# Performance work log

Measured on AMD Instinct MI355X. Metric: run time of the kernel, lower is better.

The kernel has to match this reference:

```python
import jax, jax.numpy as jnp
import numpy as np

D_MODEL = 1024
N_HEADS = 16
D_HEAD = D_MODEL // N_HEADS
D_FF = 4096
EPS = 1e-5


def layernorm(x, gamma, beta):
    mu = jnp.mean(x, axis=-1, keepdims=True)
    var = jnp.var(x, axis=-1, keepdims=True)
    return (x - mu) * jax.lax.rsqrt(var + EPS) * gamma + beta


def setup_inputs() -> dict:
    key = jax.random.key(0)
    ks = jax.random.split(key, 16)
    B, T = 4, 2048
    s = 1.0 / np.sqrt(D_MODEL)
    sf = 1.0 / np.sqrt(D_FF)
    return {
        "x": jax.random.normal(ks[0], (B, T, D_MODEL), jnp.float32),
        "gate_score": jax.random.uniform(ks[1], (B,), jnp.float32),
        "Wq": jax.random.normal(ks[2], (D_MODEL, D_MODEL), jnp.float32) * s,
        "bq": jnp.zeros((D_MODEL,), jnp.float32),
        "Wk": jax.random.normal(ks[3], (D_MODEL, D_MODEL), jnp.float32) * s,
        "bk": jnp.zeros((D_MODEL,), jnp.float32),
        "Wv": jax.random.normal(ks[4], (D_MODEL, D_MODEL), jnp.float32) * s,
        "bv": jnp.zeros((D_MODEL,), jnp.float32),
        "Wo": jax.random.normal(ks[5], (D_MODEL, D_MODEL), jnp.float32) * s,
        "bo": jnp.zeros((D_MODEL,), jnp.float32),
        "W1": jax.random.normal(ks[6], (D_MODEL, D_FF), jnp.float32) * s,
        "b1": jnp.zeros((D_FF,), jnp.float32),
        "W2": jax.random.normal(ks[7], (D_FF, D_MODEL), jnp.float32) * sf,
        "b2": jnp.zeros((D_MODEL,), jnp.float32),
        "gamma1": jnp.ones((D_MODEL,), jnp.float32),
        "beta1": jnp.zeros((D_MODEL,), jnp.float32),
        "gamma2": jnp.ones((D_MODEL,), jnp.float32),
        "beta2": jnp.zeros((D_MODEL,), jnp.float32),
    }


def reference(x, gate_score, Wq, bq, Wk, bk, Wv, bv, Wo, bo,
              W1, b1, W2, b2, gamma1, beta1, gamma2, beta2):
    B, T, C = x.shape
    # --- attention sub-block (pre-norm) ---
    h = layernorm(x, gamma1, beta1)
    Q = (h @ Wq + bq).reshape(B, T, N_HEADS, D_HEAD).transpose(0, 2, 1, 3)
    K = (h @ Wk + bk).reshape(B, T, N_HEADS, D_HEAD).transpose(0, 2, 1, 3)
    V = (h @ Wv + bv).reshape(B, T, N_HEADS, D_HEAD).transpose(0, 2, 1, 3)
    scores = jnp.einsum("bhqd,bhkd->bhqk", Q, K) / np.sqrt(D_HEAD)
    causal = jnp.tril(jnp.ones((T, T), dtype=bool))  # True = keep
    scores = jnp.where(causal, scores, -jnp.inf)
    attn = jax.nn.softmax(scores, axis=-1)
    ctx = jnp.einsum("bhqk,bhkd->bhqd", attn, V)
    ctx = ctx.transpose(0, 2, 1, 3).reshape(B, T, C)
    attn_out = ctx @ Wo + bo
    x1 = x + attn_out
    # --- FFN sub-block (pre-norm) ---
    h2 = layernorm(x1, gamma2, beta2)
    ff = jax.nn.gelu(h2 @ W1 + b1, approximate=False) @ W2 + b2
    x2 = x1 + ff
    # --- gated residual ---
    g = gate_score[:, None, None]
    return x + g * (x2 - x)
```

## Files before the change

### kernel.cpp

```cpp
#include <hip/hip_runtime.h>
#include <hip/hip_bf16.h>
#include <cmath>

typedef unsigned short u16;
typedef __attribute__((ext_vector_type(8))) short short8;
typedef __attribute__((ext_vector_type(4))) float f32x4;

#define DM 1024
#define NH 16
#define DH 64
#define DFF 4096
#define BB 4
#define TT 2048
#define MROWS (BB*TT)

__device__ __forceinline__ float bu2f(u16 u) {
    union { float f; unsigned v; } c; c.v = ((unsigned)u) << 16; return c.f;
}
__device__ __forceinline__ u16 f2bu(float f) {
    __hip_bfloat16 h = __float2bfloat16(f);
    union { __hip_bfloat16 h; u16 u; } c; c.h = h; return c.u;
}
__device__ __forceinline__ void async_copy16(const u16* g, u16* l) {
    __builtin_amdgcn_global_load_lds((const __attribute__((address_space(1))) void*)g,
                                     (__attribute__((address_space(3))) void*)l, 16, 0, 0);
}

__global__ void ln_kernel(const float* __restrict__ x, const float* __restrict__ gamma,
                          const float* __restrict__ beta, u16* __restrict__ out)
{
    int row = blockIdx.x;
    int tid = threadIdx.x;
    float4 v4 = ((const float4*)(x + (size_t)row * DM))[tid];
    float v[4] = { v4.x, v4.y, v4.z, v4.w };
    float s = v[0] + v[1] + v[2] + v[3];
    float ss = v[0]*v[0] + v[1]*v[1] + v[2]*v[2] + v[3]*v[3];
    #pragma unroll
    for (int o = 32; o > 0; o >>= 1) { s += __shfl_down(s, o); ss += __shfl_down(ss, o); }
    __shared__ float red[8];
    int w = tid >> 6;
    if ((tid & 63) == 0) { red[w] = s; red[4 + w] = ss; }
    __syncthreads();
    s  = red[0] + red[1] + red[2] + red[3];
    ss = red[4] + red[5] + red[6] + red[7];
    float mu  = s * (1.0f / DM);
    float var = ss * (1.0f / DM) - mu * mu;
    float rstd = rsqrtf(var + 1e-5f);
    float4 g4 = ((const float4*)gamma)[tid];
    float4 b4 = ((const float4*)beta)[tid];
    float g[4] = { g4.x, g4.y, g4.z, g4.w };
    float b[4] = { b4.x, b4.y, b4.z, b4.w };
    ushort4 o4;
    u16* op = (u16*)&o4;
    #pragma unroll
    for (int i = 0; i < 4; i++) op[i] = f2bu((v[i] - mu) * rstd * g[i] + b[i]);
    ((ushort4*)(out + (size_t)row * DM))[tid] = o4;
}

__global__ void transpose_f2b(const float* __restrict__ in, u16* __restrict__ out,
                              int R, int C)
{
    __shared__ u16 tile[32][33];
    int bx = blockIdx.x * 32;
    int by = blockIdx.y * 32;
    int tx = threadIdx.x, ty = threadIdx.y;
    #pragma unroll
    for (int i = 0; i < 32; i += 8)
        tile[ty + i][tx] = f2bu(in[(size_t)(by + ty + i) * C + bx + tx]);
    __syncthreads();
    #pragma unroll
    for (int i = 0; i < 32; i += 8)
        out[(size_t)(bx + ty + i) * R + by + tx] = tile[tx][ty + i];
}

#define BM 128
#define BN 128
#define BK 32

template<int EPI>
__global__ __launch_bounds__(256, 2) void gemm_bt(
    const u16* __restrict__ A, const u16* __restrict__ Bt,
    const float* __restrict__ bias, void* __restrict__ Cv,
    const float* __restrict__ res, const float* __restrict__ x0,
    const float* __restrict__ gate, int M, int N, int K)
{
    __shared__ __align__(16) u16 As[BM * BK];
    __shared__ __align__(16) u16 Bs[BN * BK];
    int tid = threadIdx.x;
    int lane = tid & 63, wave = tid >> 6;
    int wm = (wave & 1) * 64, wn = (wave >> 1) * 64;
    int lm = lane & 15, quad = lane >> 4;
    size_t row0 = (size_t)blockIdx.x * BM;
    size_t col0 = (size_t)blockIdx.y * BN;

    int sr = tid >> 2;
    int sk = (tid & 3) * 8;
    const u16* Ag = A  + (row0 + sr) * (size_t)K + sk;
    const u16* Bg = Bt + (col0 + sr) * (size_t)K + sk;
    u16* Asl = As + tid * 8;
    u16* Bsl = Bs + tid * 8;

    f32x4 acc[4][4];
    #pragma unroll
    for (int i = 0; i < 4; i++)
        #pragma unroll
        for (int j = 0; j < 4; j++)
            acc[i][j] = (f32x4){0.f, 0.f, 0.f, 0.f};

    for (int k0 = 0; k0 < K; k0 += BK) {
        __syncthreads();
        async_copy16(Ag + k0,                  Asl);
        async_copy16(Ag + (size_t)64 * K + k0, Asl + 64 * BK);
        async_copy16(Bg + k0,                  Bsl);
        async_copy16(Bg + (size_t)64 * K + k0, Bsl + 64 * BK);
        __syncthreads();
        short8 af[4], bfr[4];
        #pragma unroll
        for (int t = 0; t < 4; t++) {
            af[t]  = *(const short8*)&As[(wm + t * 16 + lm) * BK + quad * 8];
            bfr[t] = *(const short8*)&Bs[(wn + t * 16 + lm) * BK + quad * 8];
        }
        #pragma unroll
        for (int mt = 0; mt < 4; mt++)
            #pragma unroll
            for (int nt = 0; nt < 4; nt++)
                acc[mt][nt] = __builtin_amdgcn_mfma_f32_16x16x32_bf16(
                    af[mt], bfr[nt], acc[mt][nt], 0, 0, 0);
    }

    u16*   C16 = (u16*)Cv;
    float* Cf  = (float*)Cv;

    #pragma unroll
    for (int mt = 0; mt < 4; mt++) {
        #pragma unroll
        for (int nt = 0; nt < 4; nt++) {
            #pragma unroll
            for (int r = 0; r < 4; r++) {
                size_t row = row0 + wm + mt * 16 + quad * 4 + r;
                size_t col = col0 + wn + nt * 16 + lm;
                size_t idx = row * (size_t)N + col;
                float v = acc[mt][nt][r] + bias[col];
                if (EPI == 0) {
                    C16[idx] = f2bu(v);
                } else if (EPI == 1) {
                    Cf[idx] = v + res[idx];
                } else if (EPI == 2) {
                    v = 0.5f * v * (1.0f + erff(v * 0.70710678118f));
                    C16[idx] = f2bu(v);
                } else {
                    float xv  = x0[idx];
                    float x1v = res[idx];
                    float g   = gate[row >> 11];
                    Cf[idx] = xv + g * (x1v + v - xv);
                }
            }
        }
    }
}

#define KS 72
#define VS 72

__global__ __launch_bounds__(256, 4) void attn_mfma(
    const u16* __restrict__ Q, const u16* __restrict__ Kg,
    const u16* __restrict__ Vg, u16* __restrict__ ctx)
{
    __shared__ __align__(16) u16 Kl[64][KS];
    __shared__ __align__(16) u16 Vt[80][VS];
    __shared__ __align__(16) u16 Pl[4][32][VS];

    int tid = threadIdx.x, lane = tid & 63, w = tid >> 6;
    int lm = lane & 15, quad = lane >> 4;

    int bi = blockIdx.x;
    int tile = bi & 15, h = (bi >> 4) & 15, b = bi >> 8;
    int q0 = (15 - tile) * 128;
    int qw = q0 + w * 32;

    const size_t hoff = (size_t)h * DH;
    const u16* Qp = Q  + (size_t)b * TT * DM + hoff;
    const u16* Kp = Kg + (size_t)b * TT * DM + hoff;
    const u16* Vp = Vg + (size_t)b * TT * DM + hoff;

    for (int i = tid; i < 16 * VS; i += 256) {
        int r = i / VS, c = i % VS;
        Vt[64 + r][c] = (r == 0 && c < 64) ? (u16)0x3F80 : (u16)0;
    }

    short8 aq[2][2];
    #pragma unroll
    for (int qs = 0; qs < 2; qs++)
        #pragma unroll
        for (int dc = 0; dc < 2; dc++)
            aq[qs][dc] = *(const short8*)(Qp + (size_t)(qw + qs*16 + lm) * DM + dc*32 + quad*8);

    f32x4 o[2][4], o5[2];
    #pragma unroll
    for (int qs = 0; qs < 2; qs++) {
        #pragma unroll
        for (int ds = 0; ds < 4; ds++) o[qs][ds] = (f32x4){0.f, 0.f, 0.f, 0.f};
        o5[qs] = (f32x4){0.f, 0.f, 0.f, 0.f};
    }

    int kkey = tid & 63, kdim = (tid >> 6) * 16;
    int vkey = (tid & 31) * 2, vdim = (tid >> 5) * 8;

    const float sc = 0.18033688011f;
    const float FM = 24.0f;
    int nch = q0 / 64 + 2;

    uint4 kr0 = *(const uint4*)(Kp + (size_t)kkey * DM + kdim);
    uint4 kr1 = *(const uint4*)(Kp + (size_t)kkey * DM + kdim + 8);
    uint4 vr0 = *(const uint4*)(Vp + (size_t)vkey * DM + vdim);
    uint4 vr1 = *(const uint4*)(Vp + (size_t)(vkey + 1) * DM + vdim);

    for (int c = 0; c < nch; c++) {
        int kb = c * 64;
        __syncthreads();
        *(uint4*)&Kl[kkey][kdim]     = kr0;
        *(uint4*)&Kl[kkey][kdim + 8] = kr1;
        {
            const u16* p0 = (const u16*)&vr0;
            const u16* p1 = (const u16*)&vr1;
            #pragma unroll
            for (int j = 0; j < 8; j++) {
                ushort2 pk = { p0[j], p1[j] };
                *(ushort2*)&Vt[vdim + j][vkey] = pk;
            }
        }
        __syncthreads();

        int kbn = (c + 1 < nch) ? kb + 64 : 0;
        kr0 = *(const uint4*)(Kp + (size_t)(kbn + kkey) * DM + kdim);
        kr1 = *(const uint4*)(Kp + (size_t)(kbn + kkey) * DM + kdim + 8);
        vr0 = *(const uint4*)(Vp + (size_t)(kbn + vkey) * DM + vdim);
        vr1 = *(const uint4*)(Vp + (size_t)(kbn + vkey + 1) * DM + vdim);

        if (kb <= qw + 31) {
            f32x4 s[2][4];
            #pragma unroll
            for (int qs = 0; qs < 2; qs++)
                #pragma unroll
                for (int ks = 0; ks < 4; ks++)
                    s[qs][ks] = (f32x4){0.f, 0.f, 0.f, 0.f};
            #pragma unroll
            for (int ks = 0; ks < 4; ks++) {
                short8 b0 = *(const short8*)&Kl[ks * 16 + lm][quad * 8];
                short8 b1 = *(const short8*)&Kl[ks * 16 + lm][32 + quad * 8];
                #pragma unroll
                for (int qs = 0; qs < 2; qs++) {
                    s[qs][ks] = __builtin_amdgcn_mfma_f32_16x16x32_bf16(aq[qs][0], b0, s[qs][ks], 0, 0, 0);
                    s[qs][ks] = __builtin_amdgcn_mfma_f32_16x16x32_bf16(aq[qs][1], b1, s[qs][ks], 0, 0, 0);
                }
            }

            bool maskzone = (kb + 63 > qw);
            #pragma unroll
            for (int qs = 0; qs < 2; qs++)
                #pragma unroll
                for (int ks = 0; ks < 4; ks++)
                    #pragma unroll
                    for (int r = 0; r < 4; r++) {
                        float v = s[qs][ks][r] * sc - FM;
                        if (maskzone && (kb + ks * 16 + lm > qw + qs * 16 + quad * 4 + r))
                            v = -INFINITY;
                        Pl[w][qs * 16 + quad * 4 + r][ks * 16 + lm] = f2bu(exp2f(v));
                    }

            #pragma unroll
            for (int kc = 0; kc < 2; kc++) {
                short8 ap0 = *(const short8*)&Pl[w][lm][kc * 32 + quad * 8];
                short8 ap1 = *(const short8*)&Pl[w][16 + lm][kc * 32 + quad * 8];
                #pragma unroll
                for (int ds = 0; ds < 4; ds++) {
                    short8 bv = *(const short8*)&Vt[ds * 16 + lm][kc * 32 + quad * 8];
                    o[0][ds] = __builtin_amdgcn_mfma_f32_16x16x32_bf16(ap0, bv, o[0][ds], 0, 0, 0);
                    o[1][ds] = __builtin_amdgcn_mfma_f32_16x16x32_bf16(ap1, bv, o[1][ds], 0, 0, 0);
                }
                short8 b5 = *(const short8*)&Vt[64 + lm][kc * 32 + quad * 8];
                o5[0] = __builtin_amdgcn_mfma_f32_16x16x32_bf16(ap0, b5, o5[0], 0, 0, 0);
                o5[1] = __builtin_amdgcn_mfma_f32_16x16x32_bf16(ap1, b5, o5[1], 0, 0, 0);
            }
        }
    }

    #pragma unroll
    for (int qs = 0; qs < 2; qs++) {
        float inv[4];
        #pragma unroll
        for (int r = 0; r < 4; r++)
            inv[r] = 1.0f / __shfl(o5[qs][r], lane & 48);
        #pragma unroll
        for (int ds = 0; ds < 4; ds++)
            #pragma unroll
            for (int r = 0; r < 4; r++) {
                size_t row = (size_t)(b * TT + qw + qs * 16 + quad * 4 + r);
                ctx[row * DM + hoff + ds * 16 + lm] = f2bu(o[qs][ds][r] * inv[r]);
            }
    }
}

extern "C" void kernel_launch(void* const* d_in, const int* in_sizes, int n_in,
                              void* d_out, int out_size, void* d_ws, size_t ws_size,
                              hipStream_t stream)
{
    const float* x    = (const float*)d_in[0];
    const float* gate = (const float*)d_in[1];
    const float* Wq   = (const float*)d_in[2];
    const float* bq   = (const float*)d_in[3];
    const float* Wk   = (const float*)d_in[4];
    const float* bk   = (const float*)d_in[5];
    const float* Wv   = (const float*)d_in[6];
    const float* bv   = (const float*)d_in[7];
    const float* Wo   = (const float*)d_in[8];
    const float* bo   = (const float*)d_in[9];
    const float* W1   = (const float*)d_in[10];
    const float* b1   = (const float*)d_in[11];
    const float* W2   = (const float*)d_in[12];
    const float* b2   = (const float*)d_in[13];
    const float* gamma1 = (const float*)d_in[14];
    const float* beta1  = (const float*)d_in[15];
    const float* gamma2 = (const float*)d_in[16];
    const float* beta2  = (const float*)d_in[17];
    float* out = (float*)d_out;

    char* ws = (char*)d_ws;
    const size_t MB = 1024 * 1024;
    u16* WtQ = (u16*)(ws + 0 * MB);
    u16* WtK = (u16*)(ws + 2 * MB);
    u16* WtV = (u16*)(ws + 4 * MB);
    u16* WtO = (u16*)(ws + 6 * MB);
    u16* Wt1 = (u16*)(ws + 8 * MB);
    u16* Wt2 = (u16*)(ws + 16 * MB);
    u16* h   = (u16*)(ws + 24 * MB);
    u16* ctx = (u16*)(ws + 24 * MB);
    u16* Qb  = (u16*)(ws + 40 * MB);
    u16* Kb  = (u16*)(ws + 56 * MB);
    u16* Vb  = (u16*)(ws + 72 * MB);
    float* x1 = (float*)(ws + 40 * MB);
    u16* h2  = (u16*)(ws + 72 * MB);
    u16* ff  = (u16*)(ws + 88 * MB);

    dim3 tb(32, 8);
    transpose_f2b<<<dim3(DM / 32, DM / 32), tb, 0, stream>>>(Wq, WtQ, DM, DM);
    transpose_f2b<<<dim3(DM / 32, DM / 32), tb, 0, stream>>>(Wk, WtK, DM, DM);
    transpose_f2b<<<dim3(DM / 32, DM / 32), tb, 0, stream>>>(Wv, WtV, DM, DM);
    transpose_f2b<<<dim3(DM / 32, DM / 32), tb, 0, stream>>>(Wo, WtO, DM, DM);
    transpose_f2b<<<dim3(DFF / 32, DM / 32), tb, 0, stream>>>(W1, Wt1, DM, DFF);
    transpose_f2b<<<dim3(DM / 32, DFF / 32), tb, 0, stream>>>(W2, Wt2, DFF, DM);

    ln_kernel<<<MROWS, 256, 0, stream>>>(x, gamma1, beta1, h);

    dim3 gg(MROWS / BM, DM / BN);
    gemm_bt<0><<<gg, 256, 0, stream>>>(h, WtQ, bq, Qb, nullptr, nullptr, nullptr, MROWS, DM, DM);
    gemm_bt<0><<<gg, 256, 0, stream>>>(h, WtK, bk, Kb, nullptr, nullptr, nullptr, MROWS, DM, DM);
    gemm_bt<0><<<gg, 256, 0, stream>>>(h, WtV, bv, Vb, nullptr, nullptr, nullptr, MROWS, DM, DM);

    attn_mfma<<<BB * NH * (TT / 128), 256, 0, stream>>>(Qb, Kb, Vb, ctx);

    gemm_bt<1><<<gg, 256, 0, stream>>>(ctx, WtO, bo, x1, x, nullptr, nullptr, MROWS, DM, DM);

    ln_kernel<<<MROWS, 256, 0, stream>>>(x1, gamma2, beta2, h2);

    gemm_bt<2><<<dim3(MROWS / BM, DFF / BN), 256, 0, stream>>>(h2, Wt1, b1, ff, nullptr, nullptr, nullptr, MROWS, DFF, DM);

    gemm_bt<3><<<gg, 256, 0, stream>>>(ff, Wt2, b2, out, x1, x, gate, MROWS, DM, DFF);
}
```

Before: 631.3 us.

## Fuse QKV projections into one GEMM and rebalance causal attention tiles

Merges the Q, K and V weight transposes and projections into one transpose launch and a single GEMM of width 3*DM writing an interleaved QKV buffer, with per-section bias selection in the epilogue. Attention now reads from the interleaved buffer and gives each block a complementary pair of 64-row query tiles (t and 31-t), so causal work per block is balanced. The softmax denominator now comes from an MFMA against a constant ones vector instead of an extra LDS row, and each wave handles 16 query rows. The GEMM also drops its launch_bounds occupancy hint, which may change register allocation, and the wider strided QKV layout could reduce load locality in attention.

Result: faster. 573.0 us (-9.2%).

```diff
diff --git a/kernel.cpp b/kernel.cpp
--- a/kernel.cpp
+++ b/kernel.cpp
@@ -57,6 +57,26 @@
     ((ushort4*)(out + (size_t)row * DM))[tid] = o4;
 }
 
+__global__ void transpose4_f2b(const float* __restrict__ w0, const float* __restrict__ w1,
+                               const float* __restrict__ w2, const float* __restrict__ w3,
+                               u16* __restrict__ outQKV, u16* __restrict__ outO)
+{
+    __shared__ u16 tile[32][33];
+    const float* in = (blockIdx.z == 0) ? w0 : (blockIdx.z == 1) ? w1
+                     : (blockIdx.z == 2) ? w2 : w3;
+    u16* out = (blockIdx.z < 3) ? (outQKV + (size_t)blockIdx.z * DM * DM) : outO;
+    int bx = blockIdx.x * 32;
+    int by = blockIdx.y * 32;
+    int tx = threadIdx.x, ty = threadIdx.y;
+    #pragma unroll
+    for (int i = 0; i < 32; i += 8)
+        tile[ty + i][tx] = f2bu(in[(size_t)(by + ty + i) * DM + bx + tx]);
+    __syncthreads();
+    #pragma unroll
+    for (int i = 0; i < 32; i += 8)
+        out[(size_t)(bx + ty + i) * DM + by + tx] = tile[tx][ty + i];
+}
+
 __global__ void transpose_f2b(const float* __restrict__ in, u16* __restrict__ out,
                               int R, int C)
 {
@@ -78,9 +98,10 @@
 #define BK 32
 
 template<int EPI>
-__global__ __launch_bounds__(256, 2) void gemm_bt(
+__global__ void gemm_bt(
     const u16* __restrict__ A, const u16* __restrict__ Bt,
-    const float* __restrict__ bias, void* __restrict__ Cv,
+    const float* __restrict__ bias, const float* __restrict__ bias2,
+    const float* __restrict__ bias3, void* __restrict__ Cv,
     const float* __restrict__ res, const float* __restrict__ x0,
     const float* __restrict__ gate, int M, int N, int K)
 {
@@ -131,6 +152,14 @@
     u16*   C16 = (u16*)Cv;
     float* Cf  = (float*)Cv;
 
+    const float* bb = bias;
+    size_t csub = 0;
+    if (EPI == 0 && bias2 != nullptr) {
+        size_t cbase = col0 + wn;
+        if (cbase >= 2048)      { bb = bias3; csub = 2048; }
+        else if (cbase >= 1024) { bb = bias2; csub = 1024; }
+    }
+
     #pragma unroll
     for (int mt = 0; mt < 4; mt++) {
         #pragma unroll
@@ -140,7 +169,7 @@
                 size_t row = row0 + wm + mt * 16 + quad * 4 + r;
                 size_t col = col0 + wn + nt * 16 + lm;
                 size_t idx = row * (size_t)N + col;
-                float v = acc[mt][nt][r] + bias[col];
+                float v = acc[mt][nt][r] + bb[col - csub];
                 if (EPI == 0) {
                     C16[idx] = f2bu(v);
                 } else if (EPI == 1) {
@@ -159,48 +188,33 @@
     }
 }
 
-#define KS 72
-#define VS 72
+#define AVS 72
 
 __global__ __launch_bounds__(256, 4) void attn_mfma(
-    const u16* __restrict__ Q, const u16* __restrict__ Kg,
-    const u16* __restrict__ Vg, u16* __restrict__ ctx)
-{
-    __shared__ __align__(16) u16 Kl[64][KS];
-    __shared__ __align__(16) u16 Vt[80][VS];
-    __shared__ __align__(16) u16 Pl[4][32][VS];
-
+    const u16* __restrict__ QKV, u16* __restrict__ ctx)
+{
+    __shared__ __align__(16) u16 Kl[64][AVS];
+    __shared__ __align__(16) u16 Vt[64][AVS];
+    __shared__ __align__(16) u16 Pl[4][16][AVS];
+
+    const int LD = 3 * DM;
     int tid = threadIdx.x, lane = tid & 63, w = tid >> 6;
     int lm = lane & 15, quad = lane >> 4;
 
     int bi = blockIdx.x;
-    int tile = bi & 15, h = (bi >> 4) & 15, b = bi >> 8;
-    int q0 = (15 - tile) * 128;
-    int qw = q0 + w * 32;
+    int pair = bi & 15, h = (bi >> 4) & 15, b = bi >> 8;
+    int t1 = 31 - pair, t2 = pair;
 
     const size_t hoff = (size_t)h * DH;
-    const u16* Qp = Q  + (size_t)b * TT * DM + hoff;
-    const u16* Kp = Kg + (size_t)b * TT * DM + hoff;
-    const u16* Vp = Vg + (size_t)b * TT * DM + hoff;
-
-    for (int i = tid; i < 16 * VS; i += 256) {
-        int r = i / VS, c = i % VS;
-        Vt[64 + r][c] = (r == 0 && c < 64) ? (u16)0x3F80 : (u16)0;
-    }
-
-    short8 aq[2][2];
-    #pragma unroll
-    for (int qs = 0; qs < 2; qs++)
-        #pragma unroll
-        for (int dc = 0; dc < 2; dc++)
-            aq[qs][dc] = *(const short8*)(Qp + (size_t)(qw + qs*16 + lm) * DM + dc*32 + quad*8);
-
-    f32x4 o[2][4], o5[2];
-    #pragma unroll
-    for (int qs = 0; qs < 2; qs++) {
-        #pragma unroll
-        for (int ds = 0; ds < 4; ds++) o[qs][ds] = (f32x4){0.f, 0.f, 0.f, 0.f};
-        o5[qs] = (f32x4){0.f, 0.f, 0.f, 0.f};
+    const u16* Qp = QKV + (size_t)b * TT * LD + hoff;
+    const u16* Kp = Qp + DM;
+    const u16* Vp = Qp + 2 * DM;
+
+    short8 aqA[2], aqB[2];
+    #pragma unroll
+    for (int dc = 0; dc < 2; dc++) {
+        aqA[dc] = *(const short8*)(Qp + (size_t)(t1 * 64 + w * 16 + lm) * LD + dc * 32 + quad * 8);
+        aqB[dc] = *(const short8*)(Qp + (size_t)(t2 * 64 + w * 16 + lm) * LD + dc * 32 + quad * 8);
     }
 
     int kkey = tid & 63, kdim = (tid >> 6) * 16;
@@ -208,95 +222,96 @@
 
     const float sc = 0.18033688011f;
     const float FM = 24.0f;
-    int nch = q0 / 64 + 2;
-
-    uint4 kr0 = *(const uint4*)(Kp + (size_t)kkey * DM + kdim);
-    uint4 kr1 = *(const uint4*)(Kp + (size_t)kkey * DM + kdim + 8);
-    uint4 vr0 = *(const uint4*)(Vp + (size_t)vkey * DM + vdim);
-    uint4 vr1 = *(const uint4*)(Vp + (size_t)(vkey + 1) * DM + vdim);
-
-    for (int c = 0; c < nch; c++) {
-        int kb = c * 64;
-        __syncthreads();
-        *(uint4*)&Kl[kkey][kdim]     = kr0;
-        *(uint4*)&Kl[kkey][kdim + 8] = kr1;
-        {
-            const u16* p0 = (const u16*)&vr0;
-            const u16* p1 = (const u16*)&vr1;
-            #pragma unroll
-            for (int j = 0; j < 8; j++) {
-                ushort2 pk = { p0[j], p1[j] };
-                *(ushort2*)&Vt[vdim + j][vkey] = pk;
-            }
-        }
-        __syncthreads();
-
-        int kbn = (c + 1 < nch) ? kb + 64 : 0;
-        kr0 = *(const uint4*)(Kp + (size_t)(kbn + kkey) * DM + kdim);
-        kr1 = *(const uint4*)(Kp + (size_t)(kbn + kkey) * DM + kdim + 8);
-        vr0 = *(const uint4*)(Vp + (size_t)(kbn + vkey) * DM + vdim);
-        vr1 = *(const uint4*)(Vp + (size_t)(kbn + vkey + 1) * DM + vdim);
-
-        if (kb <= qw + 31) {
-            f32x4 s[2][4];
-            #pragma unroll
-            for (int qs = 0; qs < 2; qs++)
+    const short s1 = (short)0x3F80;
+    const short8 ones = (short8){s1, s1, s1, s1, s1, s1, s1, s1};
+
+    uint4 kr0 = *(const uint4*)(Kp + (size_t)kkey * LD + kdim);
+    uint4 kr1 = *(const uint4*)(Kp + (size_t)kkey * LD + kdim + 8);
+    uint4 vr0 = *(const uint4*)(Vp + (size_t)vkey * LD + vdim);
+    uint4 vr1 = *(const uint4*)(Vp + (size_t)(vkey + 1) * LD + vdim);
+
+    #pragma unroll
+    for (int ti = 0; ti < 2; ti++) {
+        int tcur = (ti == 0) ? t1 : t2;
+        int nch = tcur + 1;
+        int q0 = tcur * 64;
+        int qw = q0 + w * 16;
+        short8 a0 = (ti == 0) ? aqA[0] : aqB[0];
+        short8 a1 = (ti == 0) ? aqA[1] : aqB[1];
+
+        f32x4 o[4], o5;
+        #pragma unroll
+        for (int ds = 0; ds < 4; ds++) o[ds] = (f32x4){0.f, 0.f, 0.f, 0.f};
+        o5 = (f32x4){0.f, 0.f, 0.f, 0.f};
+
+        for (int c = 0; c < nch; c++) {
+            int kb = c * 64;
+            __syncthreads();
+            *(uint4*)&Kl[kkey][kdim]     = kr0;
+            *(uint4*)&Kl[kkey][kdim + 8] = kr1;
+            {
+                const u16* p0 = (const u16*)&vr0;
+                const u16* p1 = (const u16*)&vr1;
                 #pragma unroll
-                for (int ks = 0; ks < 4; ks++)
-                    s[qs][ks] = (f32x4){0.f, 0.f, 0.f, 0.f};
+                for (int j = 0; j < 8; j++) {
+                    ushort2 pk = { p0[j], p1[j] };
+                    *(ushort2*)&Vt[vdim + j][vkey] = pk;
+                }
+            }
+            __syncthreads();
+
+            {
+                int cn = (c + 1 < nch) ? (c + 1) : 0;
+                size_t kro = (size_t)(cn * 64);
+                kr0 = *(const uint4*)(Kp + (kro + kkey) * LD + kdim);
+                kr1 = *(const uint4*)(Kp + (kro + kkey) * LD + kdim + 8);
+                vr0 = *(const uint4*)(Vp + (kro + vkey) * LD + vdim);
+                vr1 = *(const uint4*)(Vp + (kro + vkey + 1) * LD + vdim);
+            }
+
+            f32x4 s[4];
+            #pragma unroll
+            for (int ks = 0; ks < 4; ks++) s[ks] = (f32x4){0.f, 0.f, 0.f, 0.f};
             #pragma unroll
             for (int ks = 0; ks < 4; ks++) {
                 short8 b0 = *(const short8*)&Kl[ks * 16 + lm][quad * 8];
                 short8 b1 = *(const short8*)&Kl[ks * 16 + lm][32 + quad * 8];
+                s[ks] = __builtin_amdgcn_mfma_f32_16x16x32_bf16(a0, b0, s[ks], 0, 0, 0);
+                s[ks] = __builtin_amdgcn_mfma_f32_16x16x32_bf16(a1, b1, s[ks], 0, 0, 0);
+            }
+
+            bool mz = (kb + 63 > qw);
+            #pragma unroll
+            for (int ks = 0; ks < 4; ks++)
                 #pragma unroll
-                for (int qs = 0; qs < 2; qs++) {
-                    s[qs][ks] = __builtin_amdgcn_mfma_f32_16x16x32_bf16(aq[qs][0], b0, s[qs][ks], 0, 0, 0);
-                    s[qs][ks] = __builtin_amdgcn_mfma_f32_16x16x32_bf16(aq[qs][1], b1, s[qs][ks], 0, 0, 0);
+                for (int r = 0; r < 4; r++) {
+                    float v = s[ks][r] * sc - FM;
+                    if (mz && (kb + ks * 16 + lm > qw + quad * 4 + r))
+                        v = -INFINITY;
+                    Pl[w][quad * 4 + r][ks * 16 + lm] = f2bu(exp2f(v));
                 }
-            }
-
-            bool maskzone = (kb + 63 > qw);
-            #pragma unroll
-            for (int qs = 0; qs < 2; qs++)
-                #pragma unroll
-                for (int ks = 0; ks < 4; ks++)
-                    #pragma unroll
-                    for (int r = 0; r < 4; r++) {
-                        float v = s[qs][ks][r] * sc - FM;
-                        if (maskzone && (kb + ks * 16 + lm > qw + qs * 16 + quad * 4 + r))
-                            v = -INFINITY;
-                        Pl[w][qs * 16 + quad * 4 + r][ks * 16 + lm] = f2bu(exp2f(v));
-                    }
 
             #pragma unroll
             for (int kc = 0; kc < 2; kc++) {
-                short8 ap0 = *(const short8*)&Pl[w][lm][kc * 32 + quad * 8];
-                short8 ap1 = *(const short8*)&Pl[w][16 + lm][kc * 32 + quad * 8];
+                short8 ap = *(const short8*)&Pl[w][lm][kc * 32 + quad * 8];
                 #pragma unroll
                 for (int ds = 0; ds < 4; ds++) {
                     short8 bv = *(const short8*)&Vt[ds * 16 + lm][kc * 32 + quad * 8];
-                    o[0][ds] = __builtin_amdgcn_mfma_f32_16x16x32_bf16(ap0, bv, o[0][ds], 0, 0, 0);
-                    o[1][ds] = __builtin_amdgcn_mfma_f32_16x16x32_bf16(ap1, bv, o[1][ds], 0, 0, 0);
+                    o[ds] = __builtin_amdgcn_mfma_f32_16x16x32_bf16(ap, bv, o[ds], 0, 0, 0);
                 }
-                short8 b5 = *(const short8*)&Vt[64 + lm][kc * 32 + quad * 8];
-                o5[0] = __builtin_amdgcn_mfma_f32_16x16x32_bf16(ap0, b5, o5[0], 0, 0, 0);
-                o5[1] = __builtin_amdgcn_mfma_f32_16x16x32_bf16(ap1, b5, o5[1], 0, 0, 0);
+                o5 = __builtin_amdgcn_mfma_f32_16x16x32_bf16(ap, ones, o5, 0, 0, 0);
             }
         }
-    }
-
-    #pragma unroll
-    for (int qs = 0; qs < 2; qs++) {
+
         float inv[4];
         #pragma unroll
-        for (int r = 0; r < 4; r++)
-            inv[r] = 1.0f / __shfl(o5[qs][r], lane & 48);
+        for (int r = 0; r < 4; r++) inv[r] = 1.0f / o5[r];
         #pragma unroll
         for (int ds = 0; ds < 4; ds++)
             #pragma unroll
             for (int r = 0; r < 4; r++) {
-                size_t row = (size_t)(b * TT + qw + qs * 16 + quad * 4 + r);
-                ctx[row * DM + hoff + ds * 16 + lm] = f2bu(o[qs][ds][r] * inv[r]);
+                size_t row = (size_t)(b * TT + qw + quad * 4 + r);
+                ctx[row * DM + hoff + ds * 16 + lm] = f2bu(o[ds][r] * inv[r]);
             }
     }
 }
@@ -327,43 +342,37 @@
 
     char* ws = (char*)d_ws;
     const size_t MB = 1024 * 1024;
-    u16* WtQ = (u16*)(ws + 0 * MB);
-    u16* WtK = (u16*)(ws + 2 * MB);
-    u16* WtV = (u16*)(ws + 4 * MB);
-    u16* WtO = (u16*)(ws + 6 * MB);
-    u16* Wt1 = (u16*)(ws + 8 * MB);
-    u16* Wt2 = (u16*)(ws + 16 * MB);
-    u16* h   = (u16*)(ws + 24 * MB);
-    u16* ctx = (u16*)(ws + 24 * MB);
-    u16* Qb  = (u16*)(ws + 40 * MB);
-    u16* Kb  = (u16*)(ws + 56 * MB);
-    u16* Vb  = (u16*)(ws + 72 * MB);
-    float* x1 = (float*)(ws + 40 * MB);
-    u16* h2  = (u16*)(ws + 72 * MB);
-    u16* ff  = (u16*)(ws + 88 * MB);
+    u16* WtQKV = (u16*)(ws + 0 * MB);
+    u16* WtO   = (u16*)(ws + 6 * MB);
+    u16* Wt1   = (u16*)(ws + 8 * MB);
+    u16* Wt2   = (u16*)(ws + 16 * MB);
+    u16* h     = (u16*)(ws + 24 * MB);
+    u16* ctx   = (u16*)(ws + 24 * MB);
+    u16* QKVb  = (u16*)(ws + 40 * MB);
+    float* x1  = (float*)(ws + 40 * MB);
+    u16* h2    = (u16*)(ws + 72 * MB);
+    u16* ff    = (u16*)(ws + 88 * MB);
 
     dim3 tb(32, 8);
-    transpose_f2b<<<dim3(DM / 32, DM / 32), tb, 0, stream>>>(Wq, WtQ, DM, DM);
-    transpose_f2b<<<dim3(DM / 32, DM / 32), tb, 0, stream>>>(Wk, WtK, DM, DM);
-    transpose_f2b<<<dim3(DM / 32, DM / 32), tb, 0, stream>>>(Wv, WtV, DM, DM);
-    transpose_f2b<<<dim3(DM / 32, DM / 32), tb, 0, stream>>>(Wo, WtO, DM, DM);
+    transpose4_f2b<<<dim3(32, 32, 4), tb, 0, stream>>>(Wq, Wk, Wv, Wo, WtQKV, WtO);
     transpose_f2b<<<dim3(DFF / 32, DM / 32), tb, 0, stream>>>(W1, Wt1, DM, DFF);
     transpose_f2b<<<dim3(DM / 32, DFF / 32), tb, 0, stream>>>(W2, Wt2, DFF, DM);
 
     ln_kernel<<<MROWS, 256, 0, stream>>>(x, gamma1, beta1, h);
 
-    dim3 gg(MROWS / BM, DM / BN);
-    gemm_bt<0><<<gg, 256, 0, stream>>>(h, WtQ, bq, Qb, nullptr, nullptr, nullptr, MROWS, DM, DM);
-    gemm_bt<0><<<gg, 256, 0, stream>>>(h, WtK, bk, Kb, nullptr, nullptr, nullptr, MROWS, DM, DM);
-    gemm_bt<0><<<gg, 256, 0, stream>>>(h, WtV, bv, Vb, nullptr, nullptr, nullptr, MROWS, DM, DM);
-
-    attn_mfma<<<BB * NH * (TT / 128), 256, 0, stream>>>(Qb, Kb, Vb, ctx);
-
-    gemm_bt<1><<<gg, 256, 0, stream>>>(ctx, WtO, bo, x1, x, nullptr, nullptr, MROWS, DM, DM);
+    gemm_bt<0><<<dim3(MROWS / BM, 3 * DM / BN), 256, 0, stream>>>(
+        h, WtQKV, bq, bk, bv, QKVb, nullptr, nullptr, nullptr, MROWS, 3 * DM, DM);
+
+    attn_mfma<<<BB * NH * 16, 256, 0, stream>>>(QKVb, ctx);
+
+    gemm_bt<1><<<dim3(MROWS / BM, DM / BN), 256, 0, stream>>>(
+        ctx, WtO, bo, nullptr, nullptr, x1, x, nullptr, nullptr, MROWS, DM, DM);
 
     ln_kernel<<<MROWS, 256, 0, stream>>>(x1, gamma2, beta2, h2);
 
-    gemm_bt<2><<<dim3(MROWS / BM, DFF / BN), 256, 0, stream>>>(h2, Wt1, b1, ff, nullptr, nullptr, nullptr, MROWS, DFF, DM);
-
-    gemm_bt<3><<<gg, 256, 0, stream>>>(ff, Wt2, b2, out, x1, x, gate, MROWS, DM, DFF);
-}
+    gemm_bt<2><<<dim3(MROWS / BM, DFF / BN), 256, 0, stream>>>(
+        h2, Wt1, b1, nullptr, nullptr, ff, nullptr, nullptr, nullptr, MROWS, DFF, DM);
+
+    gemm_bt<3><<<dim3(MROWS / BM, DM / BN), 256, 0, stream>>>(
+        ff, Wt2, b2, nullptr, nullptr, out, x1, x, gate, MROWS, DM, DFF);
+}
```
